# Performance work log

Measured on AMD Instinct MI355X. Metric: run time of the kernel, lower is better.

## Reference

```python
import jax, jax.numpy as jnp
import numpy as np

N = 100000      # nodes
E = 1000000     # edges per relation
D_IN = 128
D_OUT = 128
SLOPE = 0.2
N_REL = 3


def setup_inputs() -> dict:
    key = jax.random.key(0)
    ks = jax.random.split(key, 1 + 4 * N_REL)
    inp = {"H": jax.random.normal(ks[0], (N, D_IN), dtype=jnp.float32)}
    xav_w = float(np.sqrt(6.0 / (D_IN + D_OUT)))   # xavier_uniform bound for W
    xav_a = float(np.sqrt(6.0 / (1 + 2 * D_OUT)))  # xavier_uniform on a viewed as [1, 2d]
    for i in range(N_REL):
        inp[f"row_{i}"] = jax.random.randint(ks[1 + 4 * i], (E,), 0, N, dtype=jnp.int64)
        inp[f"col_{i}"] = jax.random.randint(ks[2 + 4 * i], (E,), 0, N, dtype=jnp.int64)
        inp[f"W_{i}"] = jax.random.uniform(ks[3 + 4 * i], (D_IN, D_OUT), jnp.float32, -xav_w, xav_w)
        inp[f"a_{i}"] = jax.random.uniform(ks[4 + 4 * i], (2 * D_OUT,), jnp.float32, -xav_a, xav_a)
    inp["bias"] = jnp.zeros((D_OUT,), jnp.float32)
    return inp


def _relation_agg(H, W, a, row, col):
    # 1) transform: Wh = H @ W_r  [N, d]
    Wh = H @ W
    d = Wh.shape[1]
    # 2) edge scores: e_ij = leaky_relu(a[:d].Wh[row] + a[d:].Wh[col])
    s_dst = Wh @ a[:d]   # coefficient for destination (row) side  [N]
    s_src = Wh @ a[d:]   # coefficient for source (col) side       [N]
    e = jax.nn.leaky_relu(s_dst[row] + s_src[col], negative_slope=SLOPE)  # [E]
    # 3) segment softmax over incoming edges of each destination node
    e_max = jax.ops.segment_max(e, row, num_segments=N)          # [N]
    e_shift = jnp.exp(e - e_max[row])                            # [E]
    e_sum = jax.ops.segment_sum(e_shift, row, num_segments=N)    # [N]
    alpha = e_shift / jnp.maximum(e_sum[row], 1e-12)             # [E]
    # 4) weighted aggregation of source features
    return jax.ops.segment_sum(alpha[:, None] * Wh[col], row, num_segments=N)  # [N, d]


def reference(H, row_0, col_0, row_1, col_1, row_2, col_2,
              W_0, W_1, W_2, a_0, a_1, a_2, bias):
    rows = (row_0, row_1, row_2)
    cols = (col_0, col_1, col_2)
    Ws = (W_0, W_1, W_2)
    As = (a_0, a_1, a_2)
    agg = jnp.zeros((N, D_OUT), H.dtype)
    for r in range(N_REL):
        agg = agg + _relation_agg(H, Ws[r], As[r], rows[r], cols[r])
    return agg + bias
```

## Files before the change

### kernel.cpp

```cpp
#include <hip/hip_runtime.h>

#define SLOPE 0.2f

typedef unsigned int uint;
typedef unsigned short ushort;
typedef __attribute__((ext_vector_type(8))) short short8;
typedef __attribute__((ext_vector_type(4))) float f32x4;

#define BINW 2048
#define BINSHIFT 11

__device__ inline ushort f2bf(float f) {
    uint u = __float_as_uint(f);
    uint r = (u + 0x7FFFu + ((u >> 16) & 1u)) >> 16;
    return (ushort)r;
}
__device__ inline uint pack2bf(float lo, float hi) {
    return (uint)f2bf(lo) | ((uint)f2bf(hi) << 16);
}
__device__ inline float bfl(uint u) { return __uint_as_float(u << 16); }
__device__ inline float bfh(uint u) { return __uint_as_float(u & 0xFFFF0000u); }

__global__ void wt3(const float* __restrict__ W0, const float* __restrict__ W1,
                    const float* __restrict__ W2, ushort* __restrict__ WT) {
    int r = blockIdx.x;
    const float* W = (r == 0) ? W0 : (r == 1) ? W1 : W2;
    ushort* wt = WT + r * 16384;
    for (int i = threadIdx.x; i < 16384; i += 256) {
        int k = i >> 7, n = i & 127;
        wt[n * 128 + k] = f2bf(W[i]);
    }
}

__global__ __launch_bounds__(256) void gemm3(const float* __restrict__ H,
                                             const ushort* __restrict__ WT,
                                             ushort* __restrict__ Wh0,
                                             ushort* __restrict__ Wh1,
                                             ushort* __restrict__ Wh2, int N) {
    __shared__ ushort lds[16384];
    const int brow = blockIdx.x * 128;
    const int t = threadIdx.x;

    for (int c = t; c < 2048; c += 256) {
        int r = c >> 4;
        int kb = (c & 15) << 4;
        int gr = brow + r;
        uint4 u = make_uint4(0, 0, 0, 0);
        if (gr < N) {
            const float* hp = H + (size_t)gr * 128 + (kb >> 1);
            float4 v0 = *reinterpret_cast<const float4*>(hp);
            float4 v1 = *reinterpret_cast<const float4*>(hp + 4);
            u.x = pack2bf(v0.x, v0.y);
            u.y = pack2bf(v0.z, v0.w);
            u.z = pack2bf(v1.x, v1.y);
            u.w = pack2bf(v1.z, v1.w);
        }
        int dst = (r << 8) + (kb ^ ((r & 7) << 4));
        *reinterpret_cast<uint4*>((char*)lds + dst) = u;
    }
    __syncthreads();

    const int wave = t >> 6, lane = t & 63;
    const int l16 = lane & 15, lhi = lane >> 4;

    for (int rel = 0; rel < 3; ++rel) {
        ushort* Wh = (rel == 0) ? Wh0 : (rel == 1) ? Wh1 : Wh2;
        const ushort* wt = WT + rel * 16384;

        short8 bf[2][4];
#pragma unroll
        for (int nt = 0; nt < 2; ++nt) {
            int n = wave * 32 + nt * 16 + l16;
#pragma unroll
            for (int ks = 0; ks < 4; ++ks)
                bf[nt][ks] = *reinterpret_cast<const short8*>(wt + n * 128 + ks * 32 + lhi * 8);
        }

        f32x4 acc[8][2];
#pragma unroll
        for (int mt = 0; mt < 8; ++mt) { acc[mt][0] = (f32x4)(0.f); acc[mt][1] = (f32x4)(0.f); }

#pragma unroll
        for (int ks = 0; ks < 4; ++ks) {
#pragma unroll
            for (int mt = 0; mt < 8; ++mt) {
                int r = mt * 16 + l16;
                int kb = (ks * 32 + lhi * 8) * 2;
                int addr = (r << 8) + (kb ^ ((r & 7) << 4));
                short8 af = *reinterpret_cast<const short8*>((char*)lds + addr);
                acc[mt][0] = __builtin_amdgcn_mfma_f32_16x16x32_bf16(af, bf[0][ks], acc[mt][0], 0, 0, 0);
                acc[mt][1] = __builtin_amdgcn_mfma_f32_16x16x32_bf16(af, bf[1][ks], acc[mt][1], 0, 0, 0);
            }
        }

#pragma unroll
        for (int mt = 0; mt < 8; ++mt)
#pragma unroll
            for (int nt = 0; nt < 2; ++nt)
#pragma unroll
                for (int reg = 0; reg < 4; ++reg) {
                    int gr = brow + mt * 16 + lhi * 4 + reg;
                    if (gr < N)
                        Wh[(size_t)gr * 128 + wave * 32 + nt * 16 + l16] = f2bf(acc[mt][nt][reg]);
                }
    }
}

__global__ __launch_bounds__(256) void scores_k(const uint* __restrict__ wh0,
                                                const uint* __restrict__ wh1,
                                                const uint* __restrict__ wh2,
                                                const float* __restrict__ a0,
                                                const float* __restrict__ a1,
                                                const float* __restrict__ a2,
                                                float* __restrict__ sd,
                                                float* __restrict__ ss, int N) {
    int node = blockIdx.x * 16 + (threadIdx.x >> 4);
    int ql = threadIdx.x & 15;
    if (node >= N) return;
#pragma unroll
    for (int r = 0; r < 3; ++r) {
        const uint* wh = (r == 0) ? wh0 : (r == 1) ? wh1 : wh2;
        const float* a = (r == 0) ? a0 : (r == 1) ? a1 : a2;
        const uint4 v = reinterpret_cast<const uint4*>(wh + ((size_t)node << 6))[ql];
        float f0 = bfl(v.x), f1 = bfh(v.x), f2 = bfl(v.y), f3 = bfh(v.y);
        float f4 = bfl(v.z), f5 = bfh(v.z), f6 = bfl(v.w), f7 = bfh(v.w);
        float4 aL0 = *reinterpret_cast<const float4*>(a + ql * 8);
        float4 aL1 = *reinterpret_cast<const float4*>(a + ql * 8 + 4);
        float4 aR0 = *reinterpret_cast<const float4*>(a + 128 + ql * 8);
        float4 aR1 = *reinterpret_cast<const float4*>(a + 128 + ql * 8 + 4);
        float pd = f0 * aL0.x + f1 * aL0.y + f2 * aL0.z + f3 * aL0.w +
                   f4 * aL1.x + f5 * aL1.y + f6 * aL1.z + f7 * aL1.w;
        float ps = f0 * aR0.x + f1 * aR0.y + f2 * aR0.z + f3 * aR0.w +
                   f4 * aR1.x + f5 * aR1.y + f6 * aR1.z + f7 * aR1.w;
#pragma unroll
        for (int off = 1; off < 16; off <<= 1) {
            pd += __shfl_xor(pd, off);
            ps += __shfl_xor(ps, off);
        }
        if (ql == 0) { sd[r * N + node] = pd; ss[r * N + node] = ps; }
    }
}

__global__ __launch_bounds__(256) void binhist(const int* __restrict__ r0,
                                               const int* __restrict__ r1,
                                               const int* __restrict__ r2,
                                               int* __restrict__ bincnt, int E, int N, int nbins) {
    __shared__ int h[256];
    int t = threadIdx.x;
    h[t] = 0;
    __syncthreads();
    int base = blockIdx.x * 4096;
#pragma unroll
    for (int k = 0; k < 16; ++k) {
        int i = base + k * 256 + t;
        if (i < 3 * E) {
            int r = (i >= 2 * E) ? 2 : (i >= E) ? 1 : 0;
            int li = i - r * E;
            const int* rp = (r == 0) ? r0 : (r == 1) ? r1 : r2;
            int idx = r * N + rp[li];
            atomicAdd(&h[idx >> BINSHIFT], 1);
        }
    }
    __syncthreads();
    if (t < nbins && h[t]) atomicAdd(&bincnt[t], h[t]);
}

__global__ __launch_bounds__(256) void binscan(const int* __restrict__ bincnt,
                                               int* __restrict__ binbase,
                                               int* __restrict__ gbincur, int nbins, int total) {
    __shared__ int sA[256], sB[256];
    int t = threadIdx.x;
    int v = (t < nbins) ? bincnt[t] : 0;
    sA[t] = v;
    __syncthreads();
    int* pa = sA; int* pb = sB;
    for (int off = 1; off < 256; off <<= 1) {
        int x = pa[t] + ((t >= off) ? pa[t - off] : 0);
        pb[t] = x;
        __syncthreads();
        int* tmp = pa; pa = pb; pb = tmp;
    }
    if (t < nbins) {
        int excl = pa[t] - v;
        binbase[t] = excl;
        gbincur[t] = excl;
    }
    if (t == 0) binbase[nbins] = total;
}

__global__ __launch_bounds__(256) void binscatter(const int* __restrict__ r0, const int* __restrict__ r1,
                                                  const int* __restrict__ r2, const int* __restrict__ c0,
                                                  const int* __restrict__ c1, const int* __restrict__ c2,
                                                  const float* __restrict__ sd, const float* __restrict__ ss,
                                                  int* __restrict__ gbincur, uint2* __restrict__ binned,
                                                  int E, int N, int nbins) {
    __shared__ uint2 staged[4096];
    __shared__ int hist[256], sB[256], curi[256], gbase[256];
    const int t = threadIdx.x;
    hist[t] = 0;
    __syncthreads();

    uint2 rec[16];
    short bn[16];
    const int base = blockIdx.x * 4096;
#pragma unroll
    for (int k = 0; k < 16; ++k) {
        int i = base + k * 256 + t;
        bn[k] = -1;
        if (i < 3 * E) {
            int r = (i >= 2 * E) ? 2 : (i >= E) ? 1 : 0;
            int li = i - r * E;
            const int* rp = (r == 0) ? r0 : (r == 1) ? r1 : r2;
            const int* cp = (r == 0) ? c0 : (r == 1) ? c1 : c2;
            int rr = rp[li], cc = cp[li];
            int idx = r * N + rr;
            int b = idx >> BINSHIFT;
            uint lo = (uint)(idx & (BINW - 1));
            float x = sd[idx] + ss[r * N + cc];
            x = (x > 0.f) ? x : SLOPE * x;
            float w = __expf(x);
            rec[k] = make_uint2((uint)cc | (lo << 17), __float_as_uint(w));
            bn[k] = (short)b;
            atomicAdd(&hist[b], 1);
        }
    }
    __syncthreads();

    int v = hist[t];
    int* pa = hist; int* pb = sB;
    for (int off = 1; off < 256; off <<= 1) {
        int x = pa[t] + ((t >= off) ? pa[t - off] : 0);
        pb[t] = x;
        __syncthreads();
        int* tmp = pa; pa = pb; pb = tmp;
    }
    sB[t] = pa[t] - v;
    curi[t] = pa[t] - v;
    if (t < nbins && v > 0) gbase[t] = atomicAdd(&gbincur[t], v);
    __syncthreads();

#pragma unroll
    for (int k = 0; k < 16; ++k)
        if (bn[k] >= 0) {
            int p = atomicAdd(&curi[bn[k]], 1);
            staged[p] = rec[k];
        }
    __syncthreads();

    const int wave = t >> 6, lane = t & 63;
    for (int b = wave; b < nbins; b += 4) {
        int s = sB[b];
        int len = hist[b] - s;
        if (len <= 0) continue;
        int g = gbase[b];
        for (int j = lane; j < len; j += 64) binned[g + j] = staged[s + j];
    }
}

__global__ __launch_bounds__(256) void binsort(const uint2* __restrict__ binned,
                                               const int* __restrict__ binbase,
                                               uint2* __restrict__ wc, int* __restrict__ offs, int L) {
    __shared__ int s1[BINW], s2[BINW];
    const int b = blockIdx.x, t = threadIdx.x;
    const int start = binbase[b], end = binbase[b + 1];
    const int ibase = b << BINSHIFT;
    const int width = min(BINW, L - ibase);

    for (int i = t; i < BINW; i += 256) s1[i] = 0;
    __syncthreads();
    for (int j = start + t; j < end; j += 256) {
        uint lo = (binned[j].x >> 17) & (BINW - 1);
        atomicAdd(&s1[lo], 1);
    }
    __syncthreads();

    int* pa = s1; int* pb = s2;
    for (int off = 1; off < BINW; off <<= 1) {
        for (int i = t; i < BINW; i += 256)
            pb[i] = pa[i] + ((i >= off) ? pa[i - off] : 0);
        __syncthreads();
        int* tmp = pa; pa = pb; pb = tmp;
    }
    for (int i = t; i < width; i += 256) offs[ibase + i] = start + pa[i];
    for (int i = t; i < BINW; i += 256) pb[i] = i ? pa[i - 1] : 0;
    __syncthreads();

    for (int j = start + t; j < end; j += 256) {
        uint2 r = binned[j];
        uint lo = (r.x >> 17) & (BINW - 1);
        int p = atomicAdd(&pb[lo], 1);
        wc[start + p] = make_uint2(r.y, r.x & 0x1FFFFu);
    }
}

__global__ __launch_bounds__(256) void aggregate3(const uint* __restrict__ wh0,
                                                  const uint* __restrict__ wh1,
                                                  const uint* __restrict__ wh2,
                                                  const uint2* __restrict__ wc,
                                                  const int* __restrict__ offs,
                                                  const float* __restrict__ bias,
                                                  float* __restrict__ out, int N) {
    int node = blockIdx.x * 16 + (threadIdx.x >> 4);
    int ql = threadIdx.x & 15;
    if (node >= N) return;

    float t0 = 0.f, t1 = 0.f, t2 = 0.f, t3 = 0.f, t4 = 0.f, t5 = 0.f, t6 = 0.f, t7 = 0.f;

#pragma unroll
    for (int r = 0; r < 3; ++r) {
        const uint* wh = (r == 0) ? wh0 : (r == 1) ? wh1 : wh2;
        int idx = r * N + node;
        int end = offs[idx];
        int beg = (idx == 0) ? 0 : offs[idx - 1];
        if (beg >= end) continue;
        float wsum = 0.f;
        float a0 = 0.f, a1 = 0.f, a2 = 0.f, a3 = 0.f, a4 = 0.f, a5 = 0.f, a6 = 0.f, a7 = 0.f;
        for (int j = beg; j < end; ++j) {
            uint2 e = wc[j];
            float w = __uint_as_float(e.x);
            int c = (int)e.y;
            uint4 v = reinterpret_cast<const uint4*>(wh + ((size_t)c << 6))[ql];
            wsum += w;
            a0 = fmaf(w, bfl(v.x), a0);
            a1 = fmaf(w, bfh(v.x), a1);
            a2 = fmaf(w, bfl(v.y), a2);
            a3 = fmaf(w, bfh(v.y), a3);
            a4 = fmaf(w, bfl(v.z), a4);
            a5 = fmaf(w, bfh(v.z), a5);
            a6 = fmaf(w, bfl(v.w), a6);
            a7 = fmaf(w, bfh(v.w), a7);
        }
        float inv = 1.f / fmaxf(wsum, 1e-12f);
        t0 = fmaf(a0, inv, t0); t1 = fmaf(a1, inv, t1);
        t2 = fmaf(a2, inv, t2); t3 = fmaf(a3, inv, t3);
        t4 = fmaf(a4, inv, t4); t5 = fmaf(a5, inv, t5);
        t6 = fmaf(a6, inv, t6); t7 = fmaf(a7, inv, t7);
    }

    float4 b0 = *reinterpret_cast<const float4*>(bias + ql * 8);
    float4 b1 = *reinterpret_cast<const float4*>(bias + ql * 8 + 4);
    float* o = out + (size_t)node * 128 + ql * 8;
    *reinterpret_cast<float4*>(o) = make_float4(t0 + b0.x, t1 + b0.y, t2 + b0.z, t3 + b0.w);
    *reinterpret_cast<float4*>(o + 4) = make_float4(t4 + b1.x, t5 + b1.y, t6 + b1.z, t7 + b1.w);
}

extern "C" void kernel_launch(void* const* d_in, const int* in_sizes, int n_in,
                              void* d_out, int out_size, void* d_ws, size_t ws_size,
                              hipStream_t stream) {
    const float* H = (const float*)d_in[0];
    const int* row[3] = {(const int*)d_in[1], (const int*)d_in[5], (const int*)d_in[9]};
    const int* col[3] = {(const int*)d_in[2], (const int*)d_in[6], (const int*)d_in[10]};
    const float* W[3] = {(const float*)d_in[3], (const float*)d_in[7], (const float*)d_in[11]};
    const float* a[3] = {(const float*)d_in[4], (const float*)d_in[8], (const float*)d_in[12]};
    const float* bias = (const float*)d_in[13];

    const int N = in_sizes[0] / 128;
    const int E = in_sizes[1];
    float* out = (float*)d_out;

    const int L = 3 * N;
    const int nbins = (L + BINW - 1) >> BINSHIFT;

    char* ws = (char*)d_ws;
    size_t off = 0;
    auto alloc = [&](size_t bytes) -> void* {
        void* p = ws + off;
        off += (bytes + 255) & ~(size_t)255;
        return p;
    };

    ushort* WT = (ushort*)alloc(3 * 16384 * 2);
    ushort* Wh[3];
    for (int r = 0; r < 3; ++r) Wh[r] = (ushort*)alloc((size_t)N * 128 * 2);
    float* sd = (float*)alloc((size_t)L * 4);
    float* ss = (float*)alloc((size_t)L * 4);
    int* offs = (int*)alloc((size_t)L * 4);
    int* bincnt = (int*)alloc((size_t)(nbins + 2) * 4);
    int* binbase = (int*)alloc((size_t)(nbins + 2) * 4);
    int* gbincur = (int*)alloc((size_t)(nbins + 2) * 4);
    uint2* wc = (uint2*)alloc((size_t)3 * E * 8);
    uint2* binned = (uint2*)d_out;

    const int nbG = (N + 127) / 128;
    const int nbQ = (N + 15) / 16;
    const int nbB = (3 * E + 4095) / 4096;

    wt3<<<3, 256, 0, stream>>>(W[0], W[1], W[2], WT);
    gemm3<<<nbG, 256, 0, stream>>>(H, WT, Wh[0], Wh[1], Wh[2], N);
    scores_k<<<nbQ, 256, 0, stream>>>((const uint*)Wh[0], (const uint*)Wh[1], (const uint*)Wh[2],
                                      a[0], a[1], a[2], sd, ss, N);

    hipMemsetAsync(bincnt, 0, (size_t)(nbins + 2) * 4, stream);
    binhist<<<nbB, 256, 0, stream>>>(row[0], row[1], row[2], bincnt, E, N, nbins);
    binscan<<<1, 256, 0, stream>>>(bincnt, binbase, gbincur, nbins, 3 * E);
    binscatter<<<nbB, 256, 0, stream>>>(row[0], row[1], row[2], col[0], col[1], col[2],
                                        sd, ss, gbincur, binned, E, N, nbins);
    binsort<<<nbins, 256, 0, stream>>>(binned, binbase, wc, offs, L);

    aggregate3<<<nbQ, 256, 0, stream>>>((const uint*)Wh[0], (const uint*)Wh[1], (const uint*)Wh[2],
                                        wc, offs, bias, out, N);
}
```

Before: 342.0 us.

## Fuse attention scores into GEMM, batch edge loads via shuffles, use nontemporal access

Attention score dot products are now computed inside the GEMM epilogue from fp32 accumulators, reduced with shuffles and LDS atomics. This removes the separate scores kernel and its re-read of the bf16 Wh arrays, and the scores now come from unrounded fp32 values. The aggregate kernel loads up to 16 edge records per group at once and broadcasts them with shuffles instead of each lane loading every record. Nontemporal loads and stores are also added to the streaming edge and output traffic, and the GEMM gains extra syncs and atomics per relation.

```diff
diff --git a/kernel.cpp b/kernel.cpp
--- a/kernel.cpp
+++ b/kernel.cpp
@@ -6,6 +6,8 @@
 typedef unsigned short ushort;
 typedef __attribute__((ext_vector_type(8))) short short8;
 typedef __attribute__((ext_vector_type(4))) float f32x4;
+typedef __attribute__((ext_vector_type(2))) uint uint2v;
+typedef __attribute__((ext_vector_type(4))) uint uint4v;
 
 #define BINW 2048
 #define BINSHIFT 11
@@ -34,10 +36,16 @@
 
 __global__ __launch_bounds__(256) void gemm3(const float* __restrict__ H,
                                              const ushort* __restrict__ WT,
+                                             const float* __restrict__ a0,
+                                             const float* __restrict__ a1,
+                                             const float* __restrict__ a2,
                                              ushort* __restrict__ Wh0,
                                              ushort* __restrict__ Wh1,
-                                             ushort* __restrict__ Wh2, int N) {
+                                             ushort* __restrict__ Wh2,
+                                             float* __restrict__ sd,
+                                             float* __restrict__ ss, int N) {
     __shared__ ushort lds[16384];
+    __shared__ float sds[128], sss[128];
     const int brow = blockIdx.x * 128;
     const int t = threadIdx.x;
 
@@ -58,6 +66,7 @@
         int dst = (r << 8) + (kb ^ ((r & 7) << 4));
         *reinterpret_cast<uint4*>((char*)lds + dst) = u;
     }
+    if (t < 128) { sds[t] = 0.f; sss[t] = 0.f; }
     __syncthreads();
 
     const int wave = t >> 6, lane = t & 63;
@@ -65,6 +74,7 @@
 
     for (int rel = 0; rel < 3; ++rel) {
         ushort* Wh = (rel == 0) ? Wh0 : (rel == 1) ? Wh1 : Wh2;
+        const float* aP = (rel == 0) ? a0 : (rel == 1) ? a1 : a2;
         const ushort* wt = WT + rel * 16384;
 
         short8 bf[2][4];
@@ -93,6 +103,27 @@
             }
         }
 
+        const int c0 = wave * 32 + l16;
+        const float aL0 = aP[c0], aL1 = aP[c0 + 16];
+        const float aR0 = aP[128 + c0], aR1 = aP[128 + c0 + 16];
+#pragma unroll
+        for (int mt = 0; mt < 8; ++mt)
+#pragma unroll
+            for (int reg = 0; reg < 4; ++reg) {
+                float pd = acc[mt][0][reg] * aL0 + acc[mt][1][reg] * aL1;
+                float ps = acc[mt][0][reg] * aR0 + acc[mt][1][reg] * aR1;
+#pragma unroll
+                for (int off = 1; off < 16; off <<= 1) {
+                    pd += __shfl_xor(pd, off);
+                    ps += __shfl_xor(ps, off);
+                }
+                if (l16 == 0) {
+                    int rloc = mt * 16 + lhi * 4 + reg;
+                    atomicAdd(&sds[rloc], pd);
+                    atomicAdd(&sss[rloc], ps);
+                }
+            }
+
 #pragma unroll
         for (int mt = 0; mt < 8; ++mt)
 #pragma unroll
@@ -103,41 +134,14 @@
                     if (gr < N)
                         Wh[(size_t)gr * 128 + wave * 32 + nt * 16 + l16] = f2bf(acc[mt][nt][reg]);
                 }
-    }
-}
-
-__global__ __launch_bounds__(256) void scores_k(const uint* __restrict__ wh0,
-                                                const uint* __restrict__ wh1,
-                                                const uint* __restrict__ wh2,
-                                                const float* __restrict__ a0,
-                                                const float* __restrict__ a1,
-                                                const float* __restrict__ a2,
-                                                float* __restrict__ sd,
-                                                float* __restrict__ ss, int N) {
-    int node = blockIdx.x * 16 + (threadIdx.x >> 4);
-    int ql = threadIdx.x & 15;
-    if (node >= N) return;
-#pragma unroll
-    for (int r = 0; r < 3; ++r) {
-        const uint* wh = (r == 0) ? wh0 : (r == 1) ? wh1 : wh2;
-        const float* a = (r == 0) ? a0 : (r == 1) ? a1 : a2;
-        const uint4 v = reinterpret_cast<const uint4*>(wh + ((size_t)node << 6))[ql];
-        float f0 = bfl(v.x), f1 = bfh(v.x), f2 = bfl(v.y), f3 = bfh(v.y);
-        float f4 = bfl(v.z), f5 = bfh(v.z), f6 = bfl(v.w), f7 = bfh(v.w);
-        float4 aL0 = *reinterpret_cast<const float4*>(a + ql * 8);
-        float4 aL1 = *reinterpret_cast<const float4*>(a + ql * 8 + 4);
-        float4 aR0 = *reinterpret_cast<const float4*>(a + 128 + ql * 8);
-        float4 aR1 = *reinterpret_cast<const float4*>(a + 128 + ql * 8 + 4);
-        float pd = f0 * aL0.x + f1 * aL0.y + f2 * aL0.z + f3 * aL0.w +
-                   f4 * aL1.x + f5 * aL1.y + f6 * aL1.z + f7 * aL1.w;
-        float ps = f0 * aR0.x + f1 * aR0.y + f2 * aR0.z + f3 * aR0.w +
-                   f4 * aR1.x + f5 * aR1.y + f6 * aR1.z + f7 * aR1.w;
-#pragma unroll
-        for (int off = 1; off < 16; off <<= 1) {
-            pd += __shfl_xor(pd, off);
-            ps += __shfl_xor(ps, off);
-        }
-        if (ql == 0) { sd[r * N + node] = pd; ss[r * N + node] = ps; }
+
+        __syncthreads();
+        if (t < 128) {
+            int gr = brow + t;
+            if (gr < N) { sd[rel * N + gr] = sds[t]; ss[rel * N + gr] = sss[t]; }
+            sds[t] = 0.f; sss[t] = 0.f;
+        }
+        __syncthreads();
     }
 }
 
@@ -157,7 +161,7 @@
             int r = (i >= 2 * E) ? 2 : (i >= E) ? 1 : 0;
             int li = i - r * E;
             const int* rp = (r == 0) ? r0 : (r == 1) ? r1 : r2;
-            int idx = r * N + rp[li];
+            int idx = r * N + __builtin_nontemporal_load(rp + li);
             atomicAdd(&h[idx >> BINSHIFT], 1);
         }
     }
@@ -192,7 +196,7 @@
                                                   const int* __restrict__ r2, const int* __restrict__ c0,
                                                   const int* __restrict__ c1, const int* __restrict__ c2,
                                                   const float* __restrict__ sd, const float* __restrict__ ss,
-                                                  int* __restrict__ gbincur, uint2* __restrict__ binned,
+                                                  int* __restrict__ gbincur, uint2v* __restrict__ binned,
                                                   int E, int N, int nbins) {
     __shared__ uint2 staged[4096];
     __shared__ int hist[256], sB[256], curi[256], gbase[256];
@@ -212,7 +216,8 @@
             int li = i - r * E;
             const int* rp = (r == 0) ? r0 : (r == 1) ? r1 : r2;
             const int* cp = (r == 0) ? c0 : (r == 1) ? c1 : c2;
-            int rr = rp[li], cc = cp[li];
+            int rr = __builtin_nontemporal_load(rp + li);
+            int cc = __builtin_nontemporal_load(cp + li);
             int idx = r * N + rr;
             int b = idx >> BINSHIFT;
             uint lo = (uint)(idx & (BINW - 1));
@@ -253,13 +258,17 @@
         int len = hist[b] - s;
         if (len <= 0) continue;
         int g = gbase[b];
-        for (int j = lane; j < len; j += 64) binned[g + j] = staged[s + j];
+        for (int j = lane; j < len; j += 64) {
+            uint2 rr = staged[s + j];
+            uint2v val; val.x = rr.x; val.y = rr.y;
+            __builtin_nontemporal_store(val, binned + g + j);
+        }
     }
 }
 
 __global__ __launch_bounds__(256) void binsort(const uint2* __restrict__ binned,
                                                const int* __restrict__ binbase,
-                                               uint2* __restrict__ wc, int* __restrict__ offs, int L) {
+                                               uint2v* __restrict__ wc, int* __restrict__ offs, int L) {
     __shared__ int s1[BINW], s2[BINW];
     const int b = blockIdx.x, t = threadIdx.x;
     const int start = binbase[b], end = binbase[b + 1];
@@ -289,19 +298,22 @@
         uint2 r = binned[j];
         uint lo = (r.x >> 17) & (BINW - 1);
         int p = atomicAdd(&pb[lo], 1);
-        wc[start + p] = make_uint2(r.y, r.x & 0x1FFFFu);
+        uint2v val; val.x = r.y; val.y = r.x & 0x1FFFFu;
+        __builtin_nontemporal_store(val, wc + start + p);
     }
 }
 
 __global__ __launch_bounds__(256) void aggregate3(const uint* __restrict__ wh0,
                                                   const uint* __restrict__ wh1,
                                                   const uint* __restrict__ wh2,
-                                                  const uint2* __restrict__ wc,
+                                                  const uint2v* __restrict__ wc,
                                                   const int* __restrict__ offs,
                                                   const float* __restrict__ bias,
                                                   float* __restrict__ out, int N) {
     int node = blockIdx.x * 16 + (threadIdx.x >> 4);
-    int ql = threadIdx.x & 15;
+    int lane = threadIdx.x & 63;
+    int ql = lane & 15;
+    int gb = lane & 48;
     if (node >= N) return;
 
     float t0 = 0.f, t1 = 0.f, t2 = 0.f, t3 = 0.f, t4 = 0.f, t5 = 0.f, t6 = 0.f, t7 = 0.f;
@@ -312,23 +324,32 @@
         int idx = r * N + node;
         int end = offs[idx];
         int beg = (idx == 0) ? 0 : offs[idx - 1];
-        if (beg >= end) continue;
+        int cnt = end - beg;
+        if (cnt <= 0) continue;
         float wsum = 0.f;
         float a0 = 0.f, a1 = 0.f, a2 = 0.f, a3 = 0.f, a4 = 0.f, a5 = 0.f, a6 = 0.f, a7 = 0.f;
-        for (int j = beg; j < end; ++j) {
-            uint2 e = wc[j];
-            float w = __uint_as_float(e.x);
-            int c = (int)e.y;
-            uint4 v = reinterpret_cast<const uint4*>(wh + ((size_t)c << 6))[ql];
-            wsum += w;
-            a0 = fmaf(w, bfl(v.x), a0);
-            a1 = fmaf(w, bfh(v.x), a1);
-            a2 = fmaf(w, bfl(v.y), a2);
-            a3 = fmaf(w, bfh(v.y), a3);
-            a4 = fmaf(w, bfl(v.z), a4);
-            a5 = fmaf(w, bfh(v.z), a5);
-            a6 = fmaf(w, bfl(v.w), a6);
-            a7 = fmaf(w, bfh(v.w), a7);
+
+        for (int base = 0; base < cnt; base += 16) {
+            int m = cnt - base; if (m > 16) m = 16;
+            uint ex = 0, ey = 0;
+            if (ql < m) {
+                uint2v e = __builtin_nontemporal_load(wc + beg + base + ql);
+                ex = e.x; ey = e.y;
+            }
+            for (int k = 0; k < m; ++k) {
+                float w = __uint_as_float((uint)__shfl((int)ex, gb + k));
+                uint cc = (uint)__shfl((int)ey, gb + k);
+                uint4v v = *(reinterpret_cast<const uint4v*>(wh + ((size_t)cc << 6)) + ql);
+                wsum += w;
+                a0 = fmaf(w, bfl(v.x), a0);
+                a1 = fmaf(w, bfh(v.x), a1);
+                a2 = fmaf(w, bfl(v.y), a2);
+                a3 = fmaf(w, bfh(v.y), a3);
+                a4 = fmaf(w, bfl(v.z), a4);
+                a5 = fmaf(w, bfh(v.z), a5);
+                a6 = fmaf(w, bfl(v.w), a6);
+                a7 = fmaf(w, bfh(v.w), a7);
+            }
         }
         float inv = 1.f / fmaxf(wsum, 1e-12f);
         t0 = fmaf(a0, inv, t0); t1 = fmaf(a1, inv, t1);
@@ -340,8 +361,10 @@
     float4 b0 = *reinterpret_cast<const float4*>(bias + ql * 8);
     float4 b1 = *reinterpret_cast<const float4*>(bias + ql * 8 + 4);
     float* o = out + (size_t)node * 128 + ql * 8;
-    *reinterpret_cast<float4*>(o) = make_float4(t0 + b0.x, t1 + b0.y, t2 + b0.z, t3 + b0.w);
-    *reinterpret_cast<float4*>(o + 4) = make_float4(t4 + b1.x, t5 + b1.y, t6 + b1.z, t7 + b1.w);
+    f32x4 o0 = {t0 + b0.x, t1 + b0.y, t2 + b0.z, t3 + b0.w};
+    f32x4 o1 = {t4 + b1.x, t5 + b1.y, t6 + b1.z, t7 + b1.w};
+    __builtin_nontemporal_store(o0, reinterpret_cast<f32x4*>(o));
+    __builtin_nontemporal_store(o1, reinterpret_cast<f32x4*>(o + 4));
 }
 
 extern "C" void kernel_launch(void* const* d_in, const int* in_sizes, int n_in,
@@ -378,24 +401,22 @@
     int* bincnt = (int*)alloc((size_t)(nbins + 2) * 4);
     int* binbase = (int*)alloc((size_t)(nbins + 2) * 4);
     int* gbincur = (int*)alloc((size_t)(nbins + 2) * 4);
-    uint2* wc = (uint2*)alloc((size_t)3 * E * 8);
-    uint2* binned = (uint2*)d_out;
+    uint2v* wc = (uint2v*)alloc((size_t)3 * E * 8);
+    uint2v* binned = (uint2v*)d_out;
 
     const int nbG = (N + 127) / 128;
     const int nbQ = (N + 15) / 16;
     const int nbB = (3 * E + 4095) / 4096;
 
     wt3<<<3, 256, 0, stream>>>(W[0], W[1], W[2], WT);
-    gemm3<<<nbG, 256, 0, stream>>>(H, WT, Wh[0], Wh[1], Wh[2], N);
-    scores_k<<<nbQ, 256, 0, stream>>>((const uint*)Wh[0], (const uint*)Wh[1], (const uint*)Wh[2],
-                                      a[0], a[1], a[2], sd, ss, N);
+    gemm3<<<nbG, 256, 0, stream>>>(H, WT, a[0], a[1], a[2], Wh[0], Wh[1], Wh[2], sd, ss, N);
 
     hipMemsetAsync(bincnt, 0, (size_t)(nbins + 2) * 4, stream);
     binhist<<<nbB, 256, 0, stream>>>(row[0], row[1], row[2], bincnt, E, N, nbins);
     binscan<<<1, 256, 0, stream>>>(bincnt, binbase, gbincur, nbins, 3 * E);
     binscatter<<<nbB, 256, 0, stream>>>(row[0], row[1], row[2], col[0], col[1], col[2],
                                         sd, ss, gbincur, binned, E, N, nbins);
-    binsort<<<nbins, 256, 0, stream>>>(binned, binbase, wc, offs, L);
+    binsort<<<nbins, 256, 0, stream>>>((const uint2*)binned, binbase, wc, offs, L);
 
     aggregate3<<<nbQ, 256, 0, stream>>>((const uint*)Wh[0], (const uint*)Wh[1], (const uint*)Wh[2],
                                         wc, offs, bias, out, N);
```

Result: slower. 426.5 us (+24.7%).
